# Kernel optimization log

Measured on AMD Instinct MI355X. Metric: run time of the kernel, lower is better.

## Reference

```python
import jax, jax.numpy as jnp
import numpy as np

N, F, H, T = 100000, 128, 128, 10
E = 1600000
NUM_GRAPHS = 512
BN_EPS = 1e-5


def setup_inputs() -> dict:
    key = jax.random.key(0)
    ks = jax.random.split(key, 16)
    x = jax.random.normal(ks[0], (N, F), dtype=jnp.float32)
    edge_index = jax.random.randint(ks[1], (2, E), 0, N, dtype=jnp.int64)
    batch = jnp.sort(jax.random.randint(ks[2], (N,), 0, NUM_GRAPHS, dtype=jnp.int64))
    s = lambda fin: 1.0 / np.sqrt(fin)
    return {
        "x": x, "edge_index": edge_index, "batch": batch,
        # GINConv 1 MLP: Linear(F,H) -> BN(H) -> ReLU -> Linear(H,H)
        "W1a": jax.random.uniform(ks[3], (F, H), jnp.float32, -s(F), s(F)),
        "b1a": jax.random.uniform(ks[4], (H,), jnp.float32, -s(F), s(F)),
        "g1": jnp.ones((H,), jnp.float32),
        "bt1": jnp.zeros((H,), jnp.float32),
        "W1b": jax.random.uniform(ks[5], (H, H), jnp.float32, -s(H), s(H)),
        "b1b": jax.random.uniform(ks[6], (H,), jnp.float32, -s(H), s(H)),
        # GINConv 2 MLP
        "W2a": jax.random.uniform(ks[7], (H, H), jnp.float32, -s(H), s(H)),
        "b2a": jax.random.uniform(ks[8], (H,), jnp.float32, -s(H), s(H)),
        "g2": jnp.ones((H,), jnp.float32),
        "bt2": jnp.zeros((H,), jnp.float32),
        "W2b": jax.random.uniform(ks[9], (H, H), jnp.float32, -s(H), s(H)),
        "b2b": jax.random.uniform(ks[10], (H,), jnp.float32, -s(H), s(H)),
        # final Linear(H, T)
        "Wl": jax.random.uniform(ks[11], (H, T), jnp.float32, -s(H), s(H)),
        "bl": jax.random.uniform(ks[12], (T,), jnp.float32, -s(H), s(H)),
    }


def _batchnorm(h, gamma, beta):
    # training-mode BN over the node dimension (biased variance), eps=1e-5
    mean = jnp.mean(h, axis=0)
    var = jnp.mean(jnp.square(h - mean), axis=0)
    return (h - mean) * jax.lax.rsqrt(var + BN_EPS) * gamma + beta


def _gin_conv(x, edge_index, Wa, ba, gamma, beta, Wb, bb):
    src, dst = edge_index[0], edge_index[1]
    # sum-aggregate neighbor messages: scatter-add x[src] into dst rows
    agg = jax.ops.segment_sum(x[src], dst, num_segments=x.shape[0])
    h = (x + agg) @ Wa + ba          # eps=0 in GINConv default
    h = jax.nn.relu(_batchnorm(h, gamma, beta))
    return h @ Wb + bb


def reference(x, edge_index, batch, W1a, b1a, g1, bt1, W1b, b1b,
              W2a, b2a, g2, bt2, W2b, b2b, Wl, bl):
    h = jax.nn.relu(_gin_conv(x, edge_index, W1a, b1a, g1, bt1, W1b, b1b))
    h = jax.nn.relu(_gin_conv(h, edge_index, W2a, b2a, g2, bt2, W2b, b2b))
    pooled = jax.ops.segment_sum(h, batch, num_segments=NUM_GRAPHS)  # [G, H]
    return pooled @ Wl + bl  # [G, T]
```

## Files before the change

### kernel.cpp

```cpp
#include <hip/hip_runtime.h>
#include <cstdint>
#include <cstddef>

#define NFEAT 128
#define TGRAPH 10
#define NGRAPHS 512
#define BN_EPS 1e-5f
#define BIN_CHUNK 2048

typedef __attribute__((ext_vector_type(8))) short bf16x8;
typedef __attribute__((ext_vector_type(4))) float f32x4;

__device__ __forceinline__ float bf2f(short s) {
    union { unsigned u; float f; } c;
    c.u = ((unsigned)(unsigned short)s) << 16;
    return c.f;
}
__device__ __forceinline__ short f2bf(float f) {
    union { float f; unsigned u; } c;
    c.f = f;
    unsigned u = c.u;
    return (short)((u + 0x7fffu + ((u >> 16) & 1u)) >> 16);
}
__device__ __forceinline__ void acc2(float& a, float& b, unsigned v) {
    union { unsigned u; float f; } lo, hi;
    lo.u = v << 16;
    hi.u = v & 0xffff0000u;
    a += lo.f;
    b += hi.f;
}

__global__ __launch_bounds__(256) void k_bucket_hist(const int* __restrict__ dst,
                                                     int* __restrict__ bhist, int E) {
    __shared__ int h[256];
    int t = threadIdx.x;
    h[t] = 0;
    __syncthreads();
    for (int e = blockIdx.x * blockDim.x + t; e < E; e += gridDim.x * blockDim.x)
        atomicAdd(&h[dst[e] >> 9], 1);
    __syncthreads();
    if (h[t]) atomicAdd(&bhist[t], h[t]);
}

__global__ void k_bucket_scan(const int* __restrict__ bhist, int* __restrict__ bbase,
                              int* __restrict__ cur256, int E) {
    __shared__ int s[256];
    int t = threadIdx.x;
    int v = bhist[t];
    s[t] = v;
    __syncthreads();
    for (int off = 1; off < 256; off <<= 1) {
        int x = 0;
        if (t >= off) x = s[t - off];
        __syncthreads();
        if (t >= off) s[t] += x;
        __syncthreads();
    }
    int excl = s[t] - v;
    bbase[t] = excl;
    cur256[t] = excl;
    if (t == 255) bbase[256] = E;
}

__global__ __launch_bounds__(256) void k_bin_scatter(const int* __restrict__ src,
                                                     const int* __restrict__ dst,
                                                     int* __restrict__ cur256,
                                                     int2* __restrict__ binned, int E) {
    __shared__ int hist[256];
    __shared__ int base[256];
    int t = threadIdx.x;
    int e0 = blockIdx.x * BIN_CHUNK;
    int e1 = min(e0 + BIN_CHUNK, E);
    hist[t] = 0;
    __syncthreads();
    for (int e = e0 + t; e < e1; e += 256) {
        int b = dst[e] >> 9;
        atomicAdd(&hist[b], 1);
    }
    __syncthreads();
    int c = hist[t];
    if (c > 0) base[t] = atomicAdd(&cur256[t], c);
    __syncthreads();
    hist[t] = 0;
    __syncthreads();
    for (int e = e0 + t; e < e1; e += 256) {
        int d = dst[e];
        int b = d >> 9;
        int loc = atomicAdd(&hist[b], 1);
        binned[base[b] + loc] = make_int2(src[e], d);
    }
}

__global__ __launch_bounds__(512) void k_bucket_csr(const int2* __restrict__ binned,
                                                    const int* __restrict__ bbase,
                                                    int* __restrict__ rowptr,
                                                    int* __restrict__ adj,
                                                    int N, int E, int nb) {
    __shared__ int deg[512];
    __shared__ int cur[512];
    int b = blockIdx.x;
    int t = threadIdx.x;
    int e0 = bbase[b], e1 = bbase[b + 1];
    deg[t] = 0;
    __syncthreads();
    for (int e = e0 + t; e < e1; e += 512)
        atomicAdd(&deg[binned[e].y & 511], 1);
    __syncthreads();
    int v = deg[t];
    for (int off = 1; off < 512; off <<= 1) {
        int x = 0;
        if (t >= off) x = deg[t - off];
        __syncthreads();
        if (t >= off) deg[t] += x;
        __syncthreads();
    }
    int excl = deg[t] - v;
    cur[t] = excl;
    int node = b * 512 + t;
    if (node < N) rowptr[node] = e0 + excl;
    if (b == nb - 1 && t == 0) rowptr[N] = E;
    __syncthreads();
    for (int e = e0 + t; e < e1; e += 512) {
        int2 p = binned[e];
        int loc = atomicAdd(&cur[p.y & 511], 1);
        adj[e0 + loc] = p.x;
    }
}

__global__ void k_prep(const float* __restrict__ x, short* __restrict__ xbf,
                       const float* __restrict__ W0, const float* __restrict__ W1,
                       const float* __restrict__ W2, const float* __restrict__ W3,
                       short* __restrict__ Wf, int n4) {
    int i = blockIdx.x * blockDim.x + threadIdx.x;
    if (i < n4) {
        float4 v = ((const float4*)x)[i];
        ushort4 o;
        o.x = (unsigned short)f2bf(v.x);
        o.y = (unsigned short)f2bf(v.y);
        o.z = (unsigned short)f2bf(v.z);
        o.w = (unsigned short)f2bf(v.w);
        ((ushort4*)xbf)[i] = o;
    } else {
        int idx = i - n4;
        if (idx < 4 * 16384) {
            int w = idx >> 14, r = idx & 16383;
            int j = r & 7, lane = (r >> 3) & 63, ct = (r >> 9) & 7, kc = r >> 12;
            int k = kc * 32 + (lane >> 4) * 8 + j;
            int n = ct * 16 + (lane & 15);
            const float* W = (w == 0) ? W0 : (w == 1) ? W1 : (w == 2) ? W2 : W3;
            Wf[idx] = f2bf(W[k * NFEAT + n]);
        }
    }
}

__global__ __launch_bounds__(256) void k_aggregate_v4(const short* __restrict__ X,
                                                      const int* __restrict__ rowptr,
                                                      const int* __restrict__ adj,
                                                      short* __restrict__ XA, int N) {
    int tid = threadIdx.x;
    int lane = tid & 63;
    int g = lane >> 4;
    int p = lane & 15;
    int wid = (blockIdx.x * blockDim.x + tid) >> 6;
    if (wid >= N) return;
    const uint4* Xv = (const uint4*)X;
    float acc[8];
#pragma unroll
    for (int j = 0; j < 8; j++) acc[j] = 0.f;
    int r0 = rowptr[wid], r1 = rowptr[wid + 1];
    for (int e = r0; e < r1; e += 8) {
        int e0 = e + g, e1 = e + 4 + g;
        uint4 v0 = {0u, 0u, 0u, 0u}, v1 = {0u, 0u, 0u, 0u};
        if (e0 < r1) v0 = Xv[(size_t)adj[e0] * 16 + p];
        if (e1 < r1) v1 = Xv[(size_t)adj[e1] * 16 + p];
        acc2(acc[0], acc[1], v0.x);
        acc2(acc[2], acc[3], v0.y);
        acc2(acc[4], acc[5], v0.z);
        acc2(acc[6], acc[7], v0.w);
        acc2(acc[0], acc[1], v1.x);
        acc2(acc[2], acc[3], v1.y);
        acc2(acc[4], acc[5], v1.z);
        acc2(acc[6], acc[7], v1.w);
    }
#pragma unroll
    for (int j = 0; j < 8; j++) {
        acc[j] += __shfl_xor(acc[j], 16);
        acc[j] += __shfl_xor(acc[j], 32);
    }
    if (g == 0) {
        uint4 sv = Xv[(size_t)wid * 16 + p];
        acc2(acc[0], acc[1], sv.x);
        acc2(acc[2], acc[3], sv.y);
        acc2(acc[4], acc[5], sv.z);
        acc2(acc[6], acc[7], sv.w);
        uint4 o;
        o.x = (unsigned)(unsigned short)f2bf(acc[0]) | ((unsigned)(unsigned short)f2bf(acc[1]) << 16);
        o.y = (unsigned)(unsigned short)f2bf(acc[2]) | ((unsigned)(unsigned short)f2bf(acc[3]) << 16);
        o.z = (unsigned)(unsigned short)f2bf(acc[4]) | ((unsigned)(unsigned short)f2bf(acc[5]) << 16);
        o.w = (unsigned)(unsigned short)f2bf(acc[6]) | ((unsigned)(unsigned short)f2bf(acc[7]) << 16);
        ((uint4*)XA)[(size_t)wid * 16 + p] = o;
    }
}

template <bool BN_RELU_IN, bool RELU_OUT, bool STATS>
__global__ __launch_bounds__(256) void k_gemm_mfma(const short* __restrict__ A,
                                                   const short* __restrict__ Wf,
                                                   const float* __restrict__ bias,
                                                   const float* __restrict__ scale,
                                                   const float* __restrict__ shift,
                                                   float* __restrict__ stats,
                                                   short* __restrict__ C, int N) {
    __shared__ float s_sum[NFEAT];
    __shared__ float s_sq[NFEAT];
    int tid = threadIdx.x;
    int wave = tid >> 6, lane = tid & 63;
    int quad = lane >> 4, l16 = lane & 15;
    int row_base = blockIdx.x * 128 + wave * 32;

    if constexpr (STATS) {
        if (tid < NFEAT) { s_sum[tid] = 0.f; s_sq[tid] = 0.f; }
        __syncthreads();
    }

    f32x4 acc[2][8];
#pragma unroll
    for (int i = 0; i < 2; i++)
#pragma unroll
        for (int j = 0; j < 8; j++) acc[i][j] = (f32x4){0.f, 0.f, 0.f, 0.f};

    int r0 = row_base + l16;
    int r1 = r0 + 16;

#pragma unroll
    for (int kc = 0; kc < 4; ++kc) {
        int koff = kc * 32 + quad * 8;
        bf16x8 a0 = {}, a1 = {};
        if (r0 < N) a0 = *(const bf16x8*)(A + (size_t)r0 * NFEAT + koff);
        if (r1 < N) a1 = *(const bf16x8*)(A + (size_t)r1 * NFEAT + koff);
        if constexpr (BN_RELU_IN) {
            float sc[8], sh[8];
            *(float4*)(sc) = *(const float4*)(scale + koff);
            *(float4*)(sc + 4) = *(const float4*)(scale + koff + 4);
            *(float4*)(sh) = *(const float4*)(shift + koff);
            *(float4*)(sh + 4) = *(const float4*)(shift + koff + 4);
#pragma unroll
            for (int j = 0; j < 8; j++) {
                float v = fmaxf(bf2f(a0[j]) * sc[j] + sh[j], 0.f);
                float u = fmaxf(bf2f(a1[j]) * sc[j] + sh[j], 0.f);
                a0[j] = f2bf(v);
                a1[j] = f2bf(u);
            }
        }
        const short* wp = Wf + ((size_t)(kc * 8) * 64 + lane) * 8;
#pragma unroll
        for (int ct = 0; ct < 8; ++ct) {
            bf16x8 b = *(const bf16x8*)(wp + (size_t)ct * 64 * 8);
            acc[0][ct] = __builtin_amdgcn_mfma_f32_16x16x32_bf16(a0, b, acc[0][ct], 0, 0, 0);
            acc[1][ct] = __builtin_amdgcn_mfma_f32_16x16x32_bf16(a1, b, acc[1][ct], 0, 0, 0);
        }
    }

#pragma unroll
    for (int ct = 0; ct < 8; ++ct) {
        int col = ct * 16 + l16;
        float bv = bias[col];
        float ls = 0.f, ls2 = 0.f;
#pragma unroll
        for (int rt = 0; rt < 2; ++rt) {
#pragma unroll
            for (int reg = 0; reg < 4; ++reg) {
                int row = row_base + rt * 16 + quad * 4 + reg;
                if (row < N) {
                    float v = acc[rt][ct][reg] + bv;
                    if constexpr (RELU_OUT) v = fmaxf(v, 0.f);
                    C[(size_t)row * NFEAT + col] = f2bf(v);
                    if constexpr (STATS) { ls += v; ls2 += v * v; }
                }
            }
        }
        if constexpr (STATS) {
            atomicAdd(&s_sum[col], ls);
            atomicAdd(&s_sq[col], ls2);
        }
    }

    if constexpr (STATS) {
        __syncthreads();
        if (tid < NFEAT) {
            atomicAdd(&stats[tid], s_sum[tid]);
            atomicAdd(&stats[NFEAT + tid], s_sq[tid]);
        }
    }
}

__global__ void k_bnfinalize(const float* __restrict__ stats, const float* __restrict__ gamma,
                             const float* __restrict__ beta, float* __restrict__ scale,
                             float* __restrict__ shift, int N) {
    int c = threadIdx.x;
    if (c < NFEAT) {
        float mean = stats[c] / (float)N;
        float var = stats[NFEAT + c] / (float)N - mean * mean;
        float inv = rsqrtf(var + BN_EPS);
        float sc = gamma[c] * inv;
        scale[c] = sc;
        shift[c] = beta[c] - mean * sc;
    }
}

__global__ __launch_bounds__(256) void k_pool2(const short* __restrict__ H2,
                                               const int* __restrict__ batch,
                                               float* __restrict__ pooled, int N) {
    int t = threadIdx.x;
    int c2 = t & 63;
    int rofs = t >> 6;
    int n0 = blockIdx.x * 128;
    int cur = -1;
    float ax = 0.f, ay = 0.f;
    for (int i = 0; i < 32; ++i) {
        int n = n0 + rofs + i * 4;
        if (n >= N) break;
        int g = batch[n];
        if (g != cur) {
            if (cur >= 0) {
                atomicAdd(&pooled[cur * NFEAT + c2 * 2], ax);
                atomicAdd(&pooled[cur * NFEAT + c2 * 2 + 1], ay);
            }
            cur = g; ax = 0.f; ay = 0.f;
        }
        unsigned v = *(const unsigned*)(H2 + (size_t)n * NFEAT + c2 * 2);
        ax += bf2f((short)(v & 0xffff));
        ay += bf2f((short)(v >> 16));
    }
    if (cur >= 0) {
        atomicAdd(&pooled[cur * NFEAT + c2 * 2], ax);
        atomicAdd(&pooled[cur * NFEAT + c2 * 2 + 1], ay);
    }
}

__global__ void k_final(const float* __restrict__ pooled, const float* __restrict__ Wl,
                        const float* __restrict__ bl, float* __restrict__ out) {
    int idx = blockIdx.x * blockDim.x + threadIdx.x;
    if (idx >= NGRAPHS * TGRAPH) return;
    int g = idx / TGRAPH, t = idx % TGRAPH;
    const float* p = pooled + (size_t)g * NFEAT;
    float acc = bl[t];
#pragma unroll 16
    for (int k = 0; k < NFEAT; ++k) acc += p[k] * Wl[k * TGRAPH + t];
    out[idx] = acc;
}

extern "C" void kernel_launch(void* const* d_in, const int* in_sizes, int n_in,
                              void* d_out, int out_size, void* d_ws, size_t ws_size,
                              hipStream_t stream) {
    const float* x = (const float*)d_in[0];
    const int* ei = (const int*)d_in[1];
    const int* batch = (const int*)d_in[2];
    const float* W1a = (const float*)d_in[3];
    const float* b1a = (const float*)d_in[4];
    const float* g1 = (const float*)d_in[5];
    const float* bt1 = (const float*)d_in[6];
    const float* W1b = (const float*)d_in[7];
    const float* b1b = (const float*)d_in[8];
    const float* W2a = (const float*)d_in[9];
    const float* b2a = (const float*)d_in[10];
    const float* g2 = (const float*)d_in[11];
    const float* bt2 = (const float*)d_in[12];
    const float* W2b = (const float*)d_in[13];
    const float* b2b = (const float*)d_in[14];
    const float* Wl = (const float*)d_in[15];
    const float* bl = (const float*)d_in[16];
    float* out = (float*)d_out;

    int N = in_sizes[2];
    int E = in_sizes[1] / 2;
    int nb = (N + 511) >> 9;
    const int* src = ei;
    const int* dst = ei + E;

    char* ws = (char*)d_ws;
    size_t off = 0;
    auto alloc = [&](size_t bytes) -> void* {
        void* p = ws + off;
        off = (off + bytes + 255) & ~(size_t)255;
        return p;
    };
    short* xbf = (short*)alloc((size_t)N * NFEAT * 2);
    short* ag = (short*)alloc((size_t)N * NFEAT * 2);
    short* ybf = (short*)alloc((size_t)N * NFEAT * 2);
    short* hbf = (short*)alloc((size_t)N * NFEAT * 2);
    short* h2bf = (short*)alloc((size_t)N * NFEAT * 2);
    short* Wf = (short*)alloc((size_t)4 * 16384 * 2);
    int* adj = (int*)alloc((size_t)E * 4);
    int2* binned = (int2*)alloc((size_t)E * 8);
    int* rowptr = (int*)alloc((size_t)(N + 1) * 4);
    int* bbase = (int*)alloc(257 * 4);
    int* cur256 = (int*)alloc(256 * 4);
    float* scale = (float*)alloc(128 * 4);
    float* shift = (float*)alloc(128 * 4);
    int* bhist = (int*)alloc(256 * 4);
    float* stats1 = (float*)alloc(256 * 4);
    float* stats2 = (float*)alloc(256 * 4);
    float* pooled = (float*)alloc((size_t)NGRAPHS * NFEAT * 4);
    size_t zbytes = (char*)(pooled + (size_t)NGRAPHS * NFEAT) - (char*)bhist;

    hipMemsetAsync(bhist, 0, zbytes, stream);

    k_bucket_hist<<<784, 256, 0, stream>>>(dst, bhist, E);
    k_bucket_scan<<<1, 256, 0, stream>>>(bhist, bbase, cur256, E);
    k_bin_scatter<<<(E + BIN_CHUNK - 1) / BIN_CHUNK, 256, 0, stream>>>(src, dst, cur256, binned, E);
    k_bucket_csr<<<nb, 512, 0, stream>>>(binned, bbase, rowptr, adj, N, E, nb);

    int n4 = N * NFEAT / 4;
    int prepTot = n4 + 4 * 16384;
    k_prep<<<(prepTot + 255) / 256, 256, 0, stream>>>(x, xbf, W1a, W1b, W2a, W2b, Wf, n4);

    int gemmBlocks = (N + 127) / 128;
    int aggBlocks = (N + 3) / 4;

    k_aggregate_v4<<<aggBlocks, 256, 0, stream>>>(xbf, rowptr, adj, ag, N);
    k_gemm_mfma<false, false, true><<<gemmBlocks, 256, 0, stream>>>(ag, Wf + 0 * 16384, b1a, nullptr, nullptr, stats1, ybf, N);
    k_bnfinalize<<<1, 128, 0, stream>>>(stats1, g1, bt1, scale, shift, N);
    k_gemm_mfma<true, true, false><<<gemmBlocks, 256, 0, stream>>>(ybf, Wf + 1 * 16384, b1b, scale, shift, nullptr, hbf, N);

    k_aggregate_v4<<<aggBlocks, 256, 0, stream>>>(hbf, rowptr, adj, ag, N);
    k_gemm_mfma<false, false, true><<<gemmBlocks, 256, 0, stream>>>(ag, Wf + 2 * 16384, b2a, nullptr, nullptr, stats2, ybf, N);
    k_bnfinalize<<<1, 128, 0, stream>>>(stats2, g2, bt2, scale, shift, N);
    k_gemm_mfma<true, true, false><<<gemmBlocks, 256, 0, stream>>>(ybf, Wf + 3 * 16384, b2b, scale, shift, nullptr, h2bf, N);

    k_pool2<<<(N + 127) / 128, 256, 0, stream>>>(h2bf, batch, pooled, N);
    k_final<<<(NGRAPHS * TGRAPH + 255) / 256, 256, 0, stream>>>(pooled, Wl, bl, out);
}
```

Baseline: 530.6 us.

## Fuse neighbor aggregation into GEMM via LDS staging and per-block BN partials

Neighbor aggregation now runs inside the first GEMM of each GIN layer: each wave aggregates its 32 rows into an LDS tile, so the intermediate aggregate buffer is no longer written and read back. All GEMMs stage their A tile and output through padded LDS rows, which gives coalesced 16-byte global loads and stores. BN statistics go to per-block partial arrays instead of global atomics, and the finalize kernel reduces over those partials. The trade-off is that aggregation now has only gemmBlocks blocks with one wave handling 32 rows in sequence, which lowers memory-level parallelism for the gather. The large LDS tile also reduces occupancy, and the single-block finalize loop over about 782 partials is serial.

```diff
diff --git a/kernel.cpp b/kernel.cpp
--- a/kernel.cpp
+++ b/kernel.cpp
@@ -7,6 +7,7 @@
 #define NGRAPHS 512
 #define BN_EPS 1e-5f
 #define BIN_CHUNK 2048
+#define ROWP 136
 
 typedef __attribute__((ext_vector_type(8))) short bf16x8;
 typedef __attribute__((ext_vector_type(4))) float f32x4;
@@ -28,6 +29,11 @@
     hi.u = v & 0xffff0000u;
     a += lo.f;
     b += hi.f;
+}
+__device__ __forceinline__ unsigned bn2(unsigned v, float scx, float shx, float scy, float shy) {
+    float a = fmaxf(bf2f((short)(v & 0xffff)) * scx + shx, 0.f);
+    float b = fmaxf(bf2f((short)(v >> 16)) * scy + shy, 0.f);
+    return (unsigned)(unsigned short)f2bf(a) | ((unsigned)(unsigned short)f2bf(b) << 16);
 }
 
 __global__ __launch_bounds__(256) void k_bucket_hist(const int* __restrict__ dst,
@@ -153,104 +159,109 @@
     }
 }
 
-__global__ __launch_bounds__(256) void k_aggregate_v4(const short* __restrict__ X,
-                                                      const int* __restrict__ rowptr,
-                                                      const int* __restrict__ adj,
-                                                      short* __restrict__ XA, int N) {
-    int tid = threadIdx.x;
-    int lane = tid & 63;
-    int g = lane >> 4;
-    int p = lane & 15;
-    int wid = (blockIdx.x * blockDim.x + tid) >> 6;
-    if (wid >= N) return;
-    const uint4* Xv = (const uint4*)X;
-    float acc[8];
-#pragma unroll
-    for (int j = 0; j < 8; j++) acc[j] = 0.f;
-    int r0 = rowptr[wid], r1 = rowptr[wid + 1];
-    for (int e = r0; e < r1; e += 8) {
-        int e0 = e + g, e1 = e + 4 + g;
-        uint4 v0 = {0u, 0u, 0u, 0u}, v1 = {0u, 0u, 0u, 0u};
-        if (e0 < r1) v0 = Xv[(size_t)adj[e0] * 16 + p];
-        if (e1 < r1) v1 = Xv[(size_t)adj[e1] * 16 + p];
-        acc2(acc[0], acc[1], v0.x);
-        acc2(acc[2], acc[3], v0.y);
-        acc2(acc[4], acc[5], v0.z);
-        acc2(acc[6], acc[7], v0.w);
-        acc2(acc[0], acc[1], v1.x);
-        acc2(acc[2], acc[3], v1.y);
-        acc2(acc[4], acc[5], v1.z);
-        acc2(acc[6], acc[7], v1.w);
-    }
-#pragma unroll
-    for (int j = 0; j < 8; j++) {
-        acc[j] += __shfl_xor(acc[j], 16);
-        acc[j] += __shfl_xor(acc[j], 32);
-    }
-    if (g == 0) {
-        uint4 sv = Xv[(size_t)wid * 16 + p];
-        acc2(acc[0], acc[1], sv.x);
-        acc2(acc[2], acc[3], sv.y);
-        acc2(acc[4], acc[5], sv.z);
-        acc2(acc[6], acc[7], sv.w);
-        uint4 o;
-        o.x = (unsigned)(unsigned short)f2bf(acc[0]) | ((unsigned)(unsigned short)f2bf(acc[1]) << 16);
-        o.y = (unsigned)(unsigned short)f2bf(acc[2]) | ((unsigned)(unsigned short)f2bf(acc[3]) << 16);
-        o.z = (unsigned)(unsigned short)f2bf(acc[4]) | ((unsigned)(unsigned short)f2bf(acc[5]) << 16);
-        o.w = (unsigned)(unsigned short)f2bf(acc[6]) | ((unsigned)(unsigned short)f2bf(acc[7]) << 16);
-        ((uint4*)XA)[(size_t)wid * 16 + p] = o;
-    }
-}
-
-template <bool BN_RELU_IN, bool RELU_OUT, bool STATS>
-__global__ __launch_bounds__(256) void k_gemm_mfma(const short* __restrict__ A,
-                                                   const short* __restrict__ Wf,
-                                                   const float* __restrict__ bias,
-                                                   const float* __restrict__ scale,
-                                                   const float* __restrict__ shift,
-                                                   float* __restrict__ stats,
-                                                   short* __restrict__ C, int N) {
+template <bool AGG, bool BN_RELU_IN, bool RELU_OUT, bool STATS>
+__global__ __launch_bounds__(256) void k_gemm(const short* __restrict__ A,
+                                              const int* __restrict__ rowptr,
+                                              const int* __restrict__ adj,
+                                              const short* __restrict__ Wf,
+                                              const float* __restrict__ bias,
+                                              const float* __restrict__ scale,
+                                              const float* __restrict__ shift,
+                                              float* __restrict__ stats_partial,
+                                              short* __restrict__ C, int N) {
+    __shared__ short a_lds[128 * ROWP];
     __shared__ float s_sum[NFEAT];
     __shared__ float s_sq[NFEAT];
     int tid = threadIdx.x;
     int wave = tid >> 6, lane = tid & 63;
     int quad = lane >> 4, l16 = lane & 15;
-    int row_base = blockIdx.x * 128 + wave * 32;
+    int lbase = wave * 32;
+    int row_base = blockIdx.x * 128 + lbase;
 
     if constexpr (STATS) {
         if (tid < NFEAT) { s_sum[tid] = 0.f; s_sq[tid] = 0.f; }
         __syncthreads();
     }
 
+    if constexpr (AGG) {
+        int g = quad, p = l16;
+        const uint4* Xv = (const uint4*)A;
+        for (int i = 0; i < 32; ++i) {
+            int grow = row_base + i;
+            if (grow >= N) break;
+            int r0 = rowptr[grow], r1 = rowptr[grow + 1];
+            float acc[8];
+#pragma unroll
+            for (int j = 0; j < 8; j++) acc[j] = 0.f;
+            for (int e = r0; e < r1; e += 8) {
+                int e0 = e + g, e1 = e + 4 + g;
+                uint4 v0 = {0u, 0u, 0u, 0u}, v1 = {0u, 0u, 0u, 0u};
+                if (e0 < r1) v0 = Xv[(size_t)adj[e0] * 16 + p];
+                if (e1 < r1) v1 = Xv[(size_t)adj[e1] * 16 + p];
+                acc2(acc[0], acc[1], v0.x);
+                acc2(acc[2], acc[3], v0.y);
+                acc2(acc[4], acc[5], v0.z);
+                acc2(acc[6], acc[7], v0.w);
+                acc2(acc[0], acc[1], v1.x);
+                acc2(acc[2], acc[3], v1.y);
+                acc2(acc[4], acc[5], v1.z);
+                acc2(acc[6], acc[7], v1.w);
+            }
+#pragma unroll
+            for (int j = 0; j < 8; j++) {
+                acc[j] += __shfl_xor(acc[j], 16);
+                acc[j] += __shfl_xor(acc[j], 32);
+            }
+            if (g == 0) {
+                uint4 sv = Xv[(size_t)grow * 16 + p];
+                acc2(acc[0], acc[1], sv.x);
+                acc2(acc[2], acc[3], sv.y);
+                acc2(acc[4], acc[5], sv.z);
+                acc2(acc[6], acc[7], sv.w);
+                uint4 o;
+                o.x = (unsigned)(unsigned short)f2bf(acc[0]) | ((unsigned)(unsigned short)f2bf(acc[1]) << 16);
+                o.y = (unsigned)(unsigned short)f2bf(acc[2]) | ((unsigned)(unsigned short)f2bf(acc[3]) << 16);
+                o.z = (unsigned)(unsigned short)f2bf(acc[4]) | ((unsigned)(unsigned short)f2bf(acc[5]) << 16);
+                o.w = (unsigned)(unsigned short)f2bf(acc[6]) | ((unsigned)(unsigned short)f2bf(acc[7]) << 16);
+                *(uint4*)(&a_lds[(lbase + i) * ROWP + p * 8]) = o;
+            }
+        }
+    } else {
+#pragma unroll
+        for (int it = 0; it < 8; ++it) {
+            int idx = it * 64 + lane;
+            int lr = idx >> 4, ch = idx & 15;
+            int grow = row_base + lr;
+            uint4 v = {0u, 0u, 0u, 0u};
+            if (grow < N) v = ((const uint4*)A)[(size_t)grow * 16 + ch];
+            if constexpr (BN_RELU_IN) {
+                int k0 = ch * 8;
+                float4 sc0 = *(const float4*)(scale + k0);
+                float4 sc1 = *(const float4*)(scale + k0 + 4);
+                float4 sh0 = *(const float4*)(shift + k0);
+                float4 sh1 = *(const float4*)(shift + k0 + 4);
+                v.x = bn2(v.x, sc0.x, sh0.x, sc0.y, sh0.y);
+                v.y = bn2(v.y, sc0.z, sh0.z, sc0.w, sh0.w);
+                v.z = bn2(v.z, sc1.x, sh1.x, sc1.y, sh1.y);
+                v.w = bn2(v.w, sc1.z, sh1.z, sc1.w, sh1.w);
+            }
+            *(uint4*)(&a_lds[(lbase + lr) * ROWP + ch * 8]) = v;
+        }
+    }
+
     f32x4 acc[2][8];
 #pragma unroll
     for (int i = 0; i < 2; i++)
 #pragma unroll
         for (int j = 0; j < 8; j++) acc[i][j] = (f32x4){0.f, 0.f, 0.f, 0.f};
 
-    int r0 = row_base + l16;
-    int r1 = r0 + 16;
-
+    const short* ap0 = &a_lds[(lbase + l16) * ROWP];
+    const short* ap1 = &a_lds[(lbase + 16 + l16) * ROWP];
 #pragma unroll
     for (int kc = 0; kc < 4; ++kc) {
         int koff = kc * 32 + quad * 8;
-        bf16x8 a0 = {}, a1 = {};
-        if (r0 < N) a0 = *(const bf16x8*)(A + (size_t)r0 * NFEAT + koff);
-        if (r1 < N) a1 = *(const bf16x8*)(A + (size_t)r1 * NFEAT + koff);
-        if constexpr (BN_RELU_IN) {
-            float sc[8], sh[8];
-            *(float4*)(sc) = *(const float4*)(scale + koff);
-            *(float4*)(sc + 4) = *(const float4*)(scale + koff + 4);
-            *(float4*)(sh) = *(const float4*)(shift + koff);
-            *(float4*)(sh + 4) = *(const float4*)(shift + koff + 4);
-#pragma unroll
-            for (int j = 0; j < 8; j++) {
-                float v = fmaxf(bf2f(a0[j]) * sc[j] + sh[j], 0.f);
-                float u = fmaxf(bf2f(a1[j]) * sc[j] + sh[j], 0.f);
-                a0[j] = f2bf(v);
-                a1[j] = f2bf(u);
-            }
-        }
+        bf16x8 a0 = *(const bf16x8*)(ap0 + koff);
+        bf16x8 a1 = *(const bf16x8*)(ap1 + koff);
         const short* wp = Wf + ((size_t)(kc * 8) * 64 + lane) * 8;
 #pragma unroll
         for (int ct = 0; ct < 8; ++ct) {
@@ -269,13 +280,14 @@
         for (int rt = 0; rt < 2; ++rt) {
 #pragma unroll
             for (int reg = 0; reg < 4; ++reg) {
-                int row = row_base + rt * 16 + quad * 4 + reg;
-                if (row < N) {
-                    float v = acc[rt][ct][reg] + bv;
+                int lrow = lbase + rt * 16 + quad * 4 + reg;
+                float v = 0.f;
+                if (row_base - lbase + lrow < N) {
+                    v = acc[rt][ct][reg] + bv;
                     if constexpr (RELU_OUT) v = fmaxf(v, 0.f);
-                    C[(size_t)row * NFEAT + col] = f2bf(v);
                     if constexpr (STATS) { ls += v; ls2 += v * v; }
                 }
+                a_lds[lrow * ROWP + col] = f2bf(v);
             }
         }
         if constexpr (STATS) {
@@ -284,27 +296,39 @@
         }
     }
 
+#pragma unroll
+    for (int it = 0; it < 8; ++it) {
+        int idx = it * 64 + lane;
+        int lr = idx >> 4, ch = idx & 15;
+        int grow = row_base + lr;
+        if (grow < N)
+            ((uint4*)C)[(size_t)grow * 16 + ch] = *(const uint4*)(&a_lds[(lbase + lr) * ROWP + ch * 8]);
+    }
+
     if constexpr (STATS) {
         __syncthreads();
         if (tid < NFEAT) {
-            atomicAdd(&stats[tid], s_sum[tid]);
-            atomicAdd(&stats[NFEAT + tid], s_sq[tid]);
-        }
-    }
-}
-
-__global__ void k_bnfinalize(const float* __restrict__ stats, const float* __restrict__ gamma,
-                             const float* __restrict__ beta, float* __restrict__ scale,
-                             float* __restrict__ shift, int N) {
+            stats_partial[(size_t)blockIdx.x * 256 + tid] = s_sum[tid];
+            stats_partial[(size_t)blockIdx.x * 256 + NFEAT + tid] = s_sq[tid];
+        }
+    }
+}
+
+__global__ void k_bnfinalize(const float* __restrict__ part, int nb,
+                             const float* __restrict__ gamma, const float* __restrict__ beta,
+                             float* __restrict__ scale, float* __restrict__ shift, int N) {
     int c = threadIdx.x;
-    if (c < NFEAT) {
-        float mean = stats[c] / (float)N;
-        float var = stats[NFEAT + c] / (float)N - mean * mean;
-        float inv = rsqrtf(var + BN_EPS);
-        float sc = gamma[c] * inv;
-        scale[c] = sc;
-        shift[c] = beta[c] - mean * sc;
-    }
+    float s = 0.f, s2 = 0.f;
+    for (int b = 0; b < nb; ++b) {
+        s += part[(size_t)b * 256 + c];
+        s2 += part[(size_t)b * 256 + NFEAT + c];
+    }
+    float mean = s / (float)N;
+    float var = s2 / (float)N - mean * mean;
+    float inv = rsqrtf(var + BN_EPS);
+    float sc = gamma[c] * inv;
+    scale[c] = sc;
+    shift[c] = beta[c] - mean * sc;
 }
 
 __global__ __launch_bounds__(256) void k_pool2(const short* __restrict__ H2,
@@ -385,7 +409,6 @@
         return p;
     };
     short* xbf = (short*)alloc((size_t)N * NFEAT * 2);
-    short* ag = (short*)alloc((size_t)N * NFEAT * 2);
     short* ybf = (short*)alloc((size_t)N * NFEAT * 2);
     short* hbf = (short*)alloc((size_t)N * NFEAT * 2);
     short* h2bf = (short*)alloc((size_t)N * NFEAT * 2);
@@ -397,9 +420,9 @@
     int* cur256 = (int*)alloc(256 * 4);
     float* scale = (float*)alloc(128 * 4);
     float* shift = (float*)alloc(128 * 4);
+    int gemmBlocks = (N + 127) / 128;
+    float* stats_partial = (float*)alloc((size_t)gemmBlocks * 256 * 4);
     int* bhist = (int*)alloc(256 * 4);
-    float* stats1 = (float*)alloc(256 * 4);
-    float* stats2 = (float*)alloc(256 * 4);
     float* pooled = (float*)alloc((size_t)NGRAPHS * NFEAT * 4);
     size_t zbytes = (char*)(pooled + (size_t)NGRAPHS * NFEAT) - (char*)bhist;
 
@@ -414,18 +437,17 @@
     int prepTot = n4 + 4 * 16384;
     k_prep<<<(prepTot + 255) / 256, 256, 0, stream>>>(x, xbf, W1a, W1b, W2a, W2b, Wf, n4);
 
-    int gemmBlocks = (N + 127) / 128;
-    int aggBlocks = (N + 3) / 4;
-
-    k_aggregate_v4<<<aggBlocks, 256, 0, stream>>>(xbf, rowptr, adj, ag, N);
-    k_gemm_mfma<false, false, true><<<gemmBlocks, 256, 0, stream>>>(ag, Wf + 0 * 16384, b1a, nullptr, nullptr, stats1, ybf, N);
-    k_bnfinalize<<<1, 128, 0, stream>>>(stats1, g1, bt1, scale, shift, N);
-    k_gemm_mfma<true, true, false><<<gemmBlocks, 256, 0, stream>>>(ybf, Wf + 1 * 16384, b1b, scale, shift, nullptr, hbf, N);
-
-    k_aggregate_v4<<<aggBlocks, 256, 0, stream>>>(hbf, rowptr, adj, ag, N);
-    k_gemm_mfma<false, false, true><<<gemmBlocks, 256, 0, stream>>>(ag, Wf + 2 * 16384, b2a, nullptr, nullptr, stats2, ybf, N);
-    k_bnfinalize<<<1, 128, 0, stream>>>(stats2, g2, bt2, scale, shift, N);
-    k_gemm_mfma<true, true, false><<<gemmBlocks, 256, 0, stream>>>(ybf, Wf + 3 * 16384, b2b, scale, shift, nullptr, h2bf, N);
+    k_gemm<true, false, false, true><<<gemmBlocks, 256, 0, stream>>>(
+        xbf, rowptr, adj, Wf + 0 * 16384, b1a, nullptr, nullptr, stats_partial, ybf, N);
+    k_bnfinalize<<<1, 128, 0, stream>>>(stats_partial, gemmBlocks, g1, bt1, scale, shift, N);
+    k_gemm<false, true, true, false><<<gemmBlocks, 256, 0, stream>>>(
+        ybf, nullptr, nullptr, Wf + 1 * 16384, b1b, scale, shift, nullptr, hbf, N);
+
+    k_gemm<true, false, false, true><<<gemmBlocks, 256, 0, stream>>>(
+        hbf, rowptr, adj, Wf + 2 * 16384, b2a, nullptr, nullptr, stats_partial, ybf, N);
+    k_bnfinalize<<<1, 128, 0, stream>>>(stats_partial, gemmBlocks, g2, bt2, scale, shift, N);
+    k_gemm<false, true, true, false><<<gemmBlocks, 256, 0, stream>>>(
+        ybf, nullptr, nullptr, Wf + 3 * 16384, b2b, scale, shift, nullptr, h2bf, N);
 
     k_pool2<<<(N + 127) / 128, 256, 0, stream>>>(h2bf, batch, pooled, N);
     k_final<<<(NGRAPHS * TGRAPH + 255) / 256, 256, 0, stream>>>(pooled, Wl, bl, out);
```

New measurement: 1.084 ms. 104% more time.

## Store GEMM inputs in MFMA fragment layout and fold BN finalize into GEMM

Applied to the files above, without the earlier changes.

The aggregation kernel and the first GEMM of each conv now write their bf16 outputs in a fragment-tiled layout matching the MFMA A-operand. The following GEMM can then read each fragment with one contiguous 16-byte load per lane, with no row bounds checks, and the intermediate buffers are padded to a multiple of 128 rows. The separate BN finalize kernel is removed: each block of the second GEMM computes scale and shift from the global stats into shared memory. This saves two launches and a global round-trip, at the cost of redundant per-block finalize work. It relies on padded rows being harmless, since they are read uninitialized and only affect rows that are never stored.

```diff
diff --git a/kernel.cpp b/kernel.cpp
--- a/kernel.cpp
+++ b/kernel.cpp
@@ -29,6 +29,7 @@
     a += lo.f;
     b += hi.f;
 }
+
 
 __global__ __launch_bounds__(256) void k_bucket_hist(const int* __restrict__ dst,
                                                      int* __restrict__ bhist, int E) {
@@ -198,27 +199,39 @@
         o.y = (unsigned)(unsigned short)f2bf(acc[2]) | ((unsigned)(unsigned short)f2bf(acc[3]) << 16);
         o.z = (unsigned)(unsigned short)f2bf(acc[4]) | ((unsigned)(unsigned short)f2bf(acc[5]) << 16);
         o.w = (unsigned)(unsigned short)f2bf(acc[6]) | ((unsigned)(unsigned short)f2bf(acc[7]) << 16);
-        ((uint4*)XA)[(size_t)wid * 16 + p] = o;
-    }
-}
-
-template <bool BN_RELU_IN, bool RELU_OUT, bool STATS>
+        size_t dst = ((size_t)(wid >> 4) * 4 + (p >> 2)) * 512 +
+                     (size_t)(((p & 3) * 16 + (wid & 15)) * 8);
+        *(uint4*)(XA + dst) = o;
+    }
+}
+
+template <bool BN_RELU_IN, bool RELU_OUT, bool STATS, bool FRAG_OUT>
 __global__ __launch_bounds__(256) void k_gemm_mfma(const short* __restrict__ A,
                                                    const short* __restrict__ Wf,
                                                    const float* __restrict__ bias,
-                                                   const float* __restrict__ scale,
-                                                   const float* __restrict__ shift,
                                                    float* __restrict__ stats,
+                                                   const float* __restrict__ gamma,
+                                                   const float* __restrict__ beta,
                                                    short* __restrict__ C, int N) {
-    __shared__ float s_sum[NFEAT];
-    __shared__ float s_sq[NFEAT];
+    __shared__ float s_aux[256];
     int tid = threadIdx.x;
     int wave = tid >> 6, lane = tid & 63;
     int quad = lane >> 4, l16 = lane & 15;
     int row_base = blockIdx.x * 128 + wave * 32;
 
     if constexpr (STATS) {
-        if (tid < NFEAT) { s_sum[tid] = 0.f; s_sq[tid] = 0.f; }
+        s_aux[tid] = 0.f;
+        __syncthreads();
+    }
+    if constexpr (BN_RELU_IN) {
+        if (tid < NFEAT) {
+            float mean = stats[tid] / (float)N;
+            float var = stats[NFEAT + tid] / (float)N - mean * mean;
+            float inv = rsqrtf(var + BN_EPS);
+            float sc = gamma[tid] * inv;
+            s_aux[tid] = sc;
+            s_aux[NFEAT + tid] = beta[tid] - mean * sc;
+        }
         __syncthreads();
     }
 
@@ -228,27 +241,20 @@
 #pragma unroll
         for (int j = 0; j < 8; j++) acc[i][j] = (f32x4){0.f, 0.f, 0.f, 0.f};
 
-    int r0 = row_base + l16;
-    int r1 = r0 + 16;
+    const short* af = A + ((size_t)(blockIdx.x * 8 + wave * 2) * 4) * 512;
 
 #pragma unroll
     for (int kc = 0; kc < 4; ++kc) {
-        int koff = kc * 32 + quad * 8;
-        bf16x8 a0 = {}, a1 = {};
-        if (r0 < N) a0 = *(const bf16x8*)(A + (size_t)r0 * NFEAT + koff);
-        if (r1 < N) a1 = *(const bf16x8*)(A + (size_t)r1 * NFEAT + koff);
+        bf16x8 a0 = *(const bf16x8*)(af + (size_t)kc * 512 + lane * 8);
+        bf16x8 a1 = *(const bf16x8*)(af + (size_t)(4 + kc) * 512 + lane * 8);
         if constexpr (BN_RELU_IN) {
-            float sc[8], sh[8];
-            *(float4*)(sc) = *(const float4*)(scale + koff);
-            *(float4*)(sc + 4) = *(const float4*)(scale + koff + 4);
-            *(float4*)(sh) = *(const float4*)(shift + koff);
-            *(float4*)(sh + 4) = *(const float4*)(shift + koff + 4);
+            int koff = kc * 32 + quad * 8;
 #pragma unroll
             for (int j = 0; j < 8; j++) {
-                float v = fmaxf(bf2f(a0[j]) * sc[j] + sh[j], 0.f);
-                float u = fmaxf(bf2f(a1[j]) * sc[j] + sh[j], 0.f);
-                a0[j] = f2bf(v);
-                a1[j] = f2bf(u);
+                float sc = s_aux[koff + j];
+                float sh = s_aux[NFEAT + koff + j];
+                a0[j] = f2bf(fmaxf(bf2f(a0[j]) * sc + sh, 0.f));
+                a1[j] = f2bf(fmaxf(bf2f(a1[j]) * sc + sh, 0.f));
             }
         }
         const short* wp = Wf + ((size_t)(kc * 8) * 64 + lane) * 8;
@@ -273,37 +279,29 @@
                 if (row < N) {
                     float v = acc[rt][ct][reg] + bv;
                     if constexpr (RELU_OUT) v = fmaxf(v, 0.f);
-                    C[(size_t)row * NFEAT + col] = f2bf(v);
+                    if constexpr (FRAG_OUT) {
+                        size_t addr = ((size_t)(row >> 4) * 4 + (col >> 5)) * 512 +
+                                      (size_t)((((col >> 3) & 3) * 16 + (row & 15)) * 8 + (col & 7));
+                        C[addr] = f2bf(v);
+                    } else {
+                        C[(size_t)row * NFEAT + col] = f2bf(v);
+                    }
                     if constexpr (STATS) { ls += v; ls2 += v * v; }
                 }
             }
         }
         if constexpr (STATS) {
-            atomicAdd(&s_sum[col], ls);
-            atomicAdd(&s_sq[col], ls2);
+            atomicAdd(&s_aux[col], ls);
+            atomicAdd(&s_aux[NFEAT + col], ls2);
         }
     }
 
     if constexpr (STATS) {
         __syncthreads();
         if (tid < NFEAT) {
-            atomicAdd(&stats[tid], s_sum[tid]);
-            atomicAdd(&stats[NFEAT + tid], s_sq[tid]);
-        }
-    }
-}
-
-__global__ void k_bnfinalize(const float* __restrict__ stats, const float* __restrict__ gamma,
-                             const float* __restrict__ beta, float* __restrict__ scale,
-                             float* __restrict__ shift, int N) {
-    int c = threadIdx.x;
-    if (c < NFEAT) {
-        float mean = stats[c] / (float)N;
-        float var = stats[NFEAT + c] / (float)N - mean * mean;
-        float inv = rsqrtf(var + BN_EPS);
-        float sc = gamma[c] * inv;
-        scale[c] = sc;
-        shift[c] = beta[c] - mean * sc;
+            atomicAdd(&stats[tid], s_aux[tid]);
+            atomicAdd(&stats[NFEAT + tid], s_aux[NFEAT + tid]);
+        }
     }
 }
 
@@ -377,6 +375,9 @@
     const int* src = ei;
     const int* dst = ei + E;
 
+    int gemmBlocks = (N + 127) / 128;
+    int padRows = gemmBlocks * 128;
+
     char* ws = (char*)d_ws;
     size_t off = 0;
     auto alloc = [&](size_t bytes) -> void* {
@@ -385,8 +386,8 @@
         return p;
     };
     short* xbf = (short*)alloc((size_t)N * NFEAT * 2);
-    short* ag = (short*)alloc((size_t)N * NFEAT * 2);
-    short* ybf = (short*)alloc((size_t)N * NFEAT * 2);
+    short* ag = (short*)alloc((size_t)padRows * NFEAT * 2);
+    short* ybf = (short*)alloc((size_t)padRows * NFEAT * 2);
     short* hbf = (short*)alloc((size_t)N * NFEAT * 2);
     short* h2bf = (short*)alloc((size_t)N * NFEAT * 2);
     short* Wf = (short*)alloc((size_t)4 * 16384 * 2);
@@ -395,8 +396,6 @@
     int* rowptr = (int*)alloc((size_t)(N + 1) * 4);
     int* bbase = (int*)alloc(257 * 4);
     int* cur256 = (int*)alloc(256 * 4);
-    float* scale = (float*)alloc(128 * 4);
-    float* shift = (float*)alloc(128 * 4);
     int* bhist = (int*)alloc(256 * 4);
     float* stats1 = (float*)alloc(256 * 4);
     float* stats2 = (float*)alloc(256 * 4);
@@ -414,18 +413,19 @@
     int prepTot = n4 + 4 * 16384;
     k_prep<<<(prepTot + 255) / 256, 256, 0, stream>>>(x, xbf, W1a, W1b, W2a, W2b, Wf, n4);
 
-    int gemmBlocks = (N + 127) / 128;
     int aggBlocks = (N + 3) / 4;
 
     k_aggregate_v4<<<aggBlocks, 256, 0, stream>>>(xbf, rowptr, adj, ag, N);
-    k_gemm_mfma<false, false, true><<<gemmBlocks, 256, 0, stream>>>(ag, Wf + 0 * 16384, b1a, nullptr, nullptr, stats1, ybf, N);
-    k_bnfinalize<<<1, 128, 0, stream>>>(stats1, g1, bt1, scale, shift, N);
-    k_gemm_mfma<true, true, false><<<gemmBlocks, 256, 0, stream>>>(ybf, Wf + 1 * 16384, b1b, scale, shift, nullptr, hbf, N);
+    k_gemm_mfma<false, false, true, true><<<gemmBlocks, 256, 0, stream>>>(
+        ag, Wf + 0 * 16384, b1a, stats1, nullptr, nullptr, ybf, N);
+    k_gemm_mfma<true, true, false, false><<<gemmBlocks, 256, 0, stream>>>(
+        ybf, Wf + 1 * 16384, b1b, stats1, g1, bt1, hbf, N);
 
     k_aggregate_v4<<<aggBlocks, 256, 0, stream>>>(hbf, rowptr, adj, ag, N);
-    k_gemm_mfma<false, false, true><<<gemmBlocks, 256, 0, stream>>>(ag, Wf + 2 * 16384, b2a, nullptr, nullptr, stats2, ybf, N);
-    k_bnfinalize<<<1, 128, 0, stream>>>(stats2, g2, bt2, scale, shift, N);
-    k_gemm_mfma<true, true, false><<<gemmBlocks, 256, 0, stream>>>(ybf, Wf + 3 * 16384, b2b, scale, shift, nullptr, h2bf, N);
+    k_gemm_mfma<false, false, true, true><<<gemmBlocks, 256, 0, stream>>>(
+        ag, Wf + 2 * 16384, b2a, stats2, nullptr, nullptr, ybf, N);
+    k_gemm_mfma<true, true, false, false><<<gemmBlocks, 256, 0, stream>>>(
+        ybf, Wf + 3 * 16384, b2b, stats2, g2, bt2, h2bf, N);
 
     k_pool2<<<(N + 127) / 128, 256, 0, stream>>>(h2bf, batch, pooled, N);
     k_final<<<(NGRAPHS * TGRAPH + 255) / 256, 256, 0, stream>>>(pooled, Wl, bl, out);
```

Result: faster. 519.3 us (-2.1%).
